# Kernel tuning notes

Measured on AMD Instinct MI355X. Metric: run time of the kernel, lower is better.

## Reference

```python
import jax, jax.numpy as jnp
import numpy as np

D_MODEL = 1024
NUM_HEADS = 16
HEAD_DIM = D_MODEL // NUM_HEADS
DILATION = 2
SEGMENT = 1024
OFFSET = 0  # head_idx % dilation_rate; head_idx derived from a random param in torch, fixed to 0 here


def setup_inputs() -> dict:
    key = jax.random.key(0)
    x = jax.random.normal(key, (4, 8192, D_MODEL), dtype=jnp.float32)
    return {"x": x}


def reference(x):
    b, n, d = x.shape  # n is already a multiple of SEGMENT (no padding needed)
    n_seg = n // SEGMENT
    k = SEGMENT // DILATION  # sparse tokens kept per segment

    # dilated gather: within each segment keep every DILATION-th token
    local_idx = OFFSET + DILATION * jnp.arange(k)                      # [k]
    global_idx = SEGMENT * jnp.arange(n_seg)[:, None] + local_idx[None, :]  # [n_seg, k]
    xs = x[:, global_idx, :]                                           # [b, n_seg, k, d]

    # multi-head self-attention within each sparse segment (q = k = v = xs)
    qh = xs.reshape(b, n_seg, k, NUM_HEADS, HEAD_DIM)
    scale = 1.0 / jnp.sqrt(jnp.asarray(HEAD_DIM, dtype=xs.dtype))
    scores = jnp.einsum('bsqhd,bskhd->bshqk', qh, qh) * scale          # [b, n_seg, h, k, k]
    attn = jax.nn.softmax(scores, axis=-1)
    seg_out = jnp.einsum('bshqk,bskhd->bsqhd', attn, qh)
    a_os = seg_out.reshape(b, n_seg * k, d)                            # [b, M, d]

    # mix_outputs: denominator-weighted scatter-add merge back to full sequence
    idx = jnp.broadcast_to(global_idx.reshape(-1), (b, n_seg * k))     # [b, M] global positions
    a_denoms = a_os.sum(axis=-1)                                       # [b, M]

    def mix(o_b, den_b, idx_b):
        sums = jnp.zeros((n,), o_b.dtype).at[idx_b].add(den_b)         # scatter_add of denoms
        alphas = den_b / sums[idx_b]                                   # gather + divide
        return jnp.zeros((n, d), o_b.dtype).at[idx_b].add(o_b * alphas[:, None])

    return jax.vmap(mix)(a_os, a_denoms, idx)                          # [b, n, d]
```

## Files before the change

### kernel.cpp

```cpp
#include <hip/hip_runtime.h>

#define DM 1024
#define NSEQ 8192

typedef __attribute__((ext_vector_type(8))) short short8;
typedef __attribute__((ext_vector_type(4))) float floatx4;

__device__ __forceinline__ unsigned pk_rn(float a, float b) {
  return __builtin_amdgcn_perm(__float_as_uint(b) + 0x8000u,
                               __float_as_uint(a) + 0x8000u, 0x07060302u);
}


__device__ __forceinline__ void build_vt(uint4* smem, int tid, int c, int buf) {
  const unsigned short* Ts = (const unsigned short*)smem;
  uint4* vb = &smem[4096 + buf * 1024];
  #pragma unroll
  for (int p = 0; p < 2; ++p) {
    int m = p * 512 + tid;
    int u16 = m >> 6, dp = m & 63;
    int d = dp ^ (u16 & 7);
    unsigned v[8];
    #pragma unroll
    for (int j = 0; j < 8; ++j) {
      int kk = c * 128 + 8 * u16 + j;
      v[j] = Ts[(kk * 8 + ((d >> 3) ^ j)) * 8 + (d & 7)];
    }
    uint4 pk;
    pk.x = v[0] | (v[1] << 16);
    pk.y = v[2] | (v[3] << 16);
    pk.z = v[4] | (v[5] << 16);
    pk.w = v[6] | (v[7] << 16);
    vb[m] = pk;
  }
}

__global__ __launch_bounds__(512, 2)
void fused_kernel(const float* __restrict__ x, float* __restrict__ out) {
  __shared__ uint4 smem[7168];
  const int tau = blockIdx.x;
  const int b = tau >> 7, s = (tau >> 4) & 7, h = tau & 15;
  const float* xb = x + ((size_t)b * NSEQ + s * 1024) * DM + h * 64;
  float* ob = out + ((size_t)b * NSEQ + s * 1024) * DM + h * 64;
  const int tid = threadIdx.x;
  const int lane = tid & 63;
  const int wu = __builtin_amdgcn_readfirstlane(tid >> 6);

  {
    const int c8 = tid & 7, rr = tid >> 3;
    float4 A[8], B[8];
    #pragma unroll
    for (int p = 0; p < 8; ++p) {
      int r = p * 64 + rr;
      const float* src = xb + (size_t)(2 * r) * DM + c8 * 8;
      A[p] = *(const float4*)src;
      B[p] = *(const float4*)(src + 4);
    }
    const float4 z = make_float4(0.f, 0.f, 0.f, 0.f);
    #pragma unroll
    for (int p = 0; p < 8; ++p) {
      int r = p * 64 + rr;
      float* zp = ob + (size_t)(2 * r + 1) * DM + c8 * 8;
      *(float4*)zp = z;
      *(float4*)(zp + 4) = z;
    }
    #pragma unroll
    for (int p = 0; p < 8; ++p) {
      int r = p * 64 + rr;
      uint4 pk;
      pk.x = pk_rn(A[p].x, A[p].y); pk.y = pk_rn(A[p].z, A[p].w);
      pk.z = pk_rn(B[p].x, B[p].y); pk.w = pk_rn(B[p].z, B[p].w);
      smem[r * 8 + (c8 ^ (r & 7))] = pk;
    }
  }
  __syncthreads();

  const int cq = lane & 15, u = lane >> 4;
  const int qw0 = wu * 64;

  short8 qf[4][2];
  #pragma unroll
  for (int qs = 0; qs < 4; ++qs) {
    int R = qw0 + qs * 16 + cq;
    #pragma unroll
    for (int ksd = 0; ksd < 2; ++ksd)
      qf[qs][ksd] = *(const short8*)&smem[R * 8 + ((4 * ksd + u) ^ (cq & 7))];
  }

  build_vt(smem, tid, 0, 0);
  __syncthreads();

  floatx4 o[4][4];
  #pragma unroll
  for (int qs = 0; qs < 4; ++qs)
    #pragma unroll
    for (int nt = 0; nt < 4; ++nt) o[qs][nt] = (floatx4){0.f, 0.f, 0.f, 0.f};
  float l[4] = {0.f, 0.f, 0.f, 0.f};
  const float cf = 0.125f * 1.44269504088896340736f;

  unsigned short* Pw = (unsigned short*)&smem[6144 + wu * 128];
  const int pswz = u ^ (cq & 3);

  for (int c = 0; c < 4; ++c) {
    if (c < 3) build_vt(smem, tid, c + 1, (c + 1) & 1);
    const uint4* vbase = &smem[4096 + (c & 1) * 1024];

    #pragma unroll
    for (int ks = 0; ks < 4; ++ks) {
      floatx4 acc[4][2];
      #pragma unroll
      for (int qs = 0; qs < 4; ++qs)
        #pragma unroll
        for (int t = 0; t < 2; ++t) acc[qs][t] = (floatx4){0.f, 0.f, 0.f, 0.f};
      #pragma unroll
      for (int t = 0; t < 2; ++t) {
        int R = c * 128 + 32 * ks + 16 * t + cq;
        #pragma unroll
        for (int ksd = 0; ksd < 2; ++ksd) {
          short8 af = *(short8*)&smem[R * 8 + ((4 * ksd + u) ^ (cq & 7))];
          #pragma unroll
          for (int qs = 0; qs < 4; ++qs)
            acc[qs][t] = __builtin_amdgcn_mfma_f32_16x16x32_bf16(af, qf[qs][ksd], acc[qs][t], 0, 0, 0);
        }
      }
      const int u16 = 4 * ks + u;
      short8 vfr[4];
      #pragma unroll
      for (int nt = 0; nt < 4; ++nt)
        vfr[nt] = *(const short8*)&vbase[u16 * 64 + 16 * nt + (cq ^ (u16 & 7))];
      #pragma unroll
      for (int qp = 0; qp < 2; ++qp) {
        #pragma unroll
        for (int q2 = 0; q2 < 2; ++q2) {
          int qs = 2 * qp + q2;
          #pragma unroll
          for (int t = 0; t < 2; ++t) {
            float p0 = __builtin_amdgcn_exp2f(acc[qs][t][0] * cf);
            float p1 = __builtin_amdgcn_exp2f(acc[qs][t][1] * cf);
            float p2 = __builtin_amdgcn_exp2f(acc[qs][t][2] * cf);
            float p3 = __builtin_amdgcn_exp2f(acc[qs][t][3] * cf);
            l[qs] += (p0 + p1) + (p2 + p3);
            uint2 w2;
            w2.x = pk_rn(p0, p1);
            w2.y = pk_rn(p2, p3);
            int unit = (q2 * 16 + cq) * 4 + ((2 * t + (u >> 1)) ^ (cq & 3));
            *(uint2*)(Pw + unit * 8 + (u & 1) * 4) = w2;
          }
        }
        #pragma unroll
        for (int q2 = 0; q2 < 2; ++q2) {
          int qs = 2 * qp + q2;
          short8 pf = *(short8*)(Pw + ((q2 * 16 + cq) * 4 + pswz) * 8);
          #pragma unroll
          for (int nt = 0; nt < 4; ++nt)
            o[qs][nt] = __builtin_amdgcn_mfma_f32_16x16x32_bf16(pf, vfr[nt], o[qs][nt], 0, 0, 0);
        }
      }
    }
    if (c < 3) __syncthreads();
  }

  #pragma unroll
  for (int qs = 0; qs < 4; ++qs) {
    float lf = l[qs];
    lf += __shfl_xor(lf, 16, 64);
    lf += __shfl_xor(lf, 32, 64);
    #pragma unroll
    for (int r = 0; r < 4; ++r) {
      float linv = 1.f / __shfl(lf, 4 * u + r, 64);
      float* orow = ob + (size_t)(2 * (qw0 + qs * 16 + 4 * u + r)) * DM + cq;
      #pragma unroll
      for (int nt = 0; nt < 4; ++nt)
        orow[nt * 16] = o[qs][nt][r] * linv;
    }
  }
}

extern "C" void kernel_launch(void* const* d_in, const int* in_sizes, int n_in,
                              void* d_out, int out_size, void* d_ws, size_t ws_size,
                              hipStream_t stream) {
  const float* x = (const float*)d_in[0];
  float* out = (float*)d_out;
  fused_kernel<<<dim3(512), dim3(512), 0, stream>>>(x, out);
}
```

Before: 293.5 us.

## Split each head-segment across two blocks with streamed double-buffered key chunks

Each (batch, segment, head) tile is now handled by two blocks, each owning half the query rows, so the grid doubles to 1024 blocks. Shared memory drops from 7168 to 4096 uint4 by keeping only two 128-row key chunks resident and streaming the rest from global memory into registers during compute. Launch bounds move to 4 blocks per CU. Each half starts at a different key chunk so the two blocks do not read the same chunk at the same time. The cost is that both halves read the full key/value set, doubling global reads of x, plus an extra barrier per chunk.

```diff
diff --git a/kernel.cpp b/kernel.cpp
--- a/kernel.cpp
+++ b/kernel.cpp
@@ -11,10 +11,8 @@
                                __float_as_uint(a) + 0x8000u, 0x07060302u);
 }
 
-
-__device__ __forceinline__ void build_vt(uint4* smem, int tid, int c, int buf) {
-  const unsigned short* Ts = (const unsigned short*)smem;
-  uint4* vb = &smem[4096 + buf * 1024];
+__device__ __forceinline__ void build_vt(uint4* smem, int tid, int bufsel) {
+  const unsigned short* Bs = (const unsigned short*)&smem[bufsel * 1024];
   #pragma unroll
   for (int p = 0; p < 2; ++p) {
     int m = p * 512 + tid;
@@ -23,103 +21,119 @@
     unsigned v[8];
     #pragma unroll
     for (int j = 0; j < 8; ++j) {
-      int kk = c * 128 + 8 * u16 + j;
-      v[j] = Ts[(kk * 8 + ((d >> 3) ^ j)) * 8 + (d & 7)];
+      int kkl = 8 * u16 + j;
+      v[j] = Bs[(kkl * 8 + ((d >> 3) ^ j)) * 8 + (d & 7)];
     }
     uint4 pk;
     pk.x = v[0] | (v[1] << 16);
     pk.y = v[2] | (v[3] << 16);
     pk.z = v[4] | (v[5] << 16);
     pk.w = v[6] | (v[7] << 16);
-    vb[m] = pk;
-  }
-}
-
-__global__ __launch_bounds__(512, 2)
-void fused_kernel(const float* __restrict__ x, float* __restrict__ out) {
-  __shared__ uint4 smem[7168];
-  const int tau = blockIdx.x;
+    smem[2048 + m] = pk;
+  }
+}
+
+__global__ __launch_bounds__(512, 4)
+void fused2(const float* __restrict__ x, float* __restrict__ out) {
+  __shared__ uint4 smem[4096];
+  const int g = blockIdx.x;
+  const int tau = (g & 7) * 64 + (g >> 4);
+  const int half = (g >> 3) & 1;
   const int b = tau >> 7, s = (tau >> 4) & 7, h = tau & 15;
   const float* xb = x + ((size_t)b * NSEQ + s * 1024) * DM + h * 64;
   float* ob = out + ((size_t)b * NSEQ + s * 1024) * DM + h * 64;
+  const int qoff = half * 256;
+  const int first = half * 2;
   const int tid = threadIdx.x;
   const int lane = tid & 63;
   const int wu = __builtin_amdgcn_readfirstlane(tid >> 6);
-
+  const int c8 = tid & 7, rr = tid >> 3;
+
+  float4 A[4], B[4];
+  #pragma unroll
+  for (int i = 0; i < 4; ++i) {
+    int rl = (i & 1) * 64 + rr;
+    int ch = first + (i >> 1);
+    const float* src = xb + (size_t)(2 * (128 * ch + rl)) * DM + c8 * 8;
+    A[i] = *(const float4*)src;
+    B[i] = *(const float4*)(src + 4);
+  }
   {
-    const int c8 = tid & 7, rr = tid >> 3;
-    float4 A[8], B[8];
-    #pragma unroll
-    for (int p = 0; p < 8; ++p) {
-      int r = p * 64 + rr;
-      const float* src = xb + (size_t)(2 * r) * DM + c8 * 8;
-      A[p] = *(const float4*)src;
-      B[p] = *(const float4*)(src + 4);
-    }
     const float4 z = make_float4(0.f, 0.f, 0.f, 0.f);
     #pragma unroll
-    for (int p = 0; p < 8; ++p) {
-      int r = p * 64 + rr;
-      float* zp = ob + (size_t)(2 * r + 1) * DM + c8 * 8;
+    for (int p = 0; p < 4; ++p) {
+      int j = qoff + p * 64 + rr;
+      float* zp = ob + (size_t)(2 * j + 1) * DM + c8 * 8;
       *(float4*)zp = z;
       *(float4*)(zp + 4) = z;
     }
-    #pragma unroll
-    for (int p = 0; p < 8; ++p) {
-      int r = p * 64 + rr;
-      uint4 pk;
-      pk.x = pk_rn(A[p].x, A[p].y); pk.y = pk_rn(A[p].z, A[p].w);
-      pk.z = pk_rn(B[p].x, B[p].y); pk.w = pk_rn(B[p].z, B[p].w);
-      smem[r * 8 + (c8 ^ (r & 7))] = pk;
-    }
+  }
+  #pragma unroll
+  for (int i = 0; i < 4; ++i) {
+    int rl = (i & 1) * 64 + rr;
+    uint4 pk;
+    pk.x = pk_rn(A[i].x, A[i].y); pk.y = pk_rn(A[i].z, A[i].w);
+    pk.z = pk_rn(B[i].x, B[i].y); pk.w = pk_rn(B[i].z, B[i].w);
+    smem[(i >> 1) * 1024 + rl * 8 + (c8 ^ (rl & 7))] = pk;
   }
   __syncthreads();
 
   const int cq = lane & 15, u = lane >> 4;
-  const int qw0 = wu * 64;
-
-  short8 qf[4][2];
-  #pragma unroll
-  for (int qs = 0; qs < 4; ++qs) {
-    int R = qw0 + qs * 16 + cq;
-    #pragma unroll
-    for (int ksd = 0; ksd < 2; ++ksd)
-      qf[qs][ksd] = *(const short8*)&smem[R * 8 + ((4 * ksd + u) ^ (cq & 7))];
-  }
-
-  build_vt(smem, tid, 0, 0);
+
+  short8 qf[2][2];
+  {
+    const uint4* bq = &smem[(wu >> 2) * 1024];
+    #pragma unroll
+    for (int qs = 0; qs < 2; ++qs) {
+      int rl = (wu & 3) * 32 + qs * 16 + cq;
+      #pragma unroll
+      for (int ksd = 0; ksd < 2; ++ksd)
+        qf[qs][ksd] = *(const short8*)&bq[rl * 8 + ((4 * ksd + u) ^ (cq & 7))];
+    }
+  }
+  build_vt(smem, tid, 0);
   __syncthreads();
 
-  floatx4 o[4][4];
-  #pragma unroll
-  for (int qs = 0; qs < 4; ++qs)
+  floatx4 o[2][4];
+  #pragma unroll
+  for (int qs = 0; qs < 2; ++qs)
     #pragma unroll
     for (int nt = 0; nt < 4; ++nt) o[qs][nt] = (floatx4){0.f, 0.f, 0.f, 0.f};
-  float l[4] = {0.f, 0.f, 0.f, 0.f};
+  float l[2] = {0.f, 0.f};
   const float cf = 0.125f * 1.44269504088896340736f;
 
-  unsigned short* Pw = (unsigned short*)&smem[6144 + wu * 128];
+  unsigned short* Pw = (unsigned short*)&smem[3072 + wu * 128];
   const int pswz = u ^ (cq & 3);
 
+  #pragma unroll
   for (int c = 0; c < 4; ++c) {
-    if (c < 3) build_vt(smem, tid, c + 1, (c + 1) & 1);
-    const uint4* vbase = &smem[4096 + (c & 1) * 1024];
+    float4 sA0, sB0, sA1, sB1;
+    if (c < 2) {
+      int ch = (first + c + 2) & 3;
+      const float* src0 = xb + (size_t)(2 * (128 * ch + rr)) * DM + c8 * 8;
+      sA0 = *(const float4*)src0;
+      sB0 = *(const float4*)(src0 + 4);
+      const float* src1 = xb + (size_t)(2 * (128 * ch + rr + 64)) * DM + c8 * 8;
+      sA1 = *(const float4*)src1;
+      sB1 = *(const float4*)(src1 + 4);
+    }
+    const uint4* kb = &smem[(c & 1) * 1024];
 
     #pragma unroll
     for (int ks = 0; ks < 4; ++ks) {
-      floatx4 acc[4][2];
-      #pragma unroll
-      for (int qs = 0; qs < 4; ++qs)
+      floatx4 acc[2][2];
+      #pragma unroll
+      for (int qs = 0; qs < 2; ++qs)
         #pragma unroll
         for (int t = 0; t < 2; ++t) acc[qs][t] = (floatx4){0.f, 0.f, 0.f, 0.f};
       #pragma unroll
       for (int t = 0; t < 2; ++t) {
-        int R = c * 128 + 32 * ks + 16 * t + cq;
+        int r = 32 * ks + 16 * t + cq;
         #pragma unroll
         for (int ksd = 0; ksd < 2; ++ksd) {
-          short8 af = *(short8*)&smem[R * 8 + ((4 * ksd + u) ^ (cq & 7))];
+          short8 af = *(const short8*)&kb[r * 8 + ((4 * ksd + u) ^ (cq & 7))];
           #pragma unroll
-          for (int qs = 0; qs < 4; ++qs)
+          for (int qs = 0; qs < 2; ++qs)
             acc[qs][t] = __builtin_amdgcn_mfma_f32_16x16x32_bf16(af, qf[qs][ksd], acc[qs][t], 0, 0, 0);
         }
       }
@@ -127,48 +141,58 @@
       short8 vfr[4];
       #pragma unroll
       for (int nt = 0; nt < 4; ++nt)
-        vfr[nt] = *(const short8*)&vbase[u16 * 64 + 16 * nt + (cq ^ (u16 & 7))];
-      #pragma unroll
-      for (int qp = 0; qp < 2; ++qp) {
-        #pragma unroll
-        for (int q2 = 0; q2 < 2; ++q2) {
-          int qs = 2 * qp + q2;
-          #pragma unroll
-          for (int t = 0; t < 2; ++t) {
-            float p0 = __builtin_amdgcn_exp2f(acc[qs][t][0] * cf);
-            float p1 = __builtin_amdgcn_exp2f(acc[qs][t][1] * cf);
-            float p2 = __builtin_amdgcn_exp2f(acc[qs][t][2] * cf);
-            float p3 = __builtin_amdgcn_exp2f(acc[qs][t][3] * cf);
-            l[qs] += (p0 + p1) + (p2 + p3);
-            uint2 w2;
-            w2.x = pk_rn(p0, p1);
-            w2.y = pk_rn(p2, p3);
-            int unit = (q2 * 16 + cq) * 4 + ((2 * t + (u >> 1)) ^ (cq & 3));
-            *(uint2*)(Pw + unit * 8 + (u & 1) * 4) = w2;
-          }
+        vfr[nt] = *(const short8*)&smem[2048 + u16 * 64 + 16 * nt + (cq ^ (u16 & 7))];
+      #pragma unroll
+      for (int qs = 0; qs < 2; ++qs)
+        #pragma unroll
+        for (int t = 0; t < 2; ++t) {
+          float p0 = __builtin_amdgcn_exp2f(acc[qs][t][0] * cf);
+          float p1 = __builtin_amdgcn_exp2f(acc[qs][t][1] * cf);
+          float p2 = __builtin_amdgcn_exp2f(acc[qs][t][2] * cf);
+          float p3 = __builtin_amdgcn_exp2f(acc[qs][t][3] * cf);
+          l[qs] += (p0 + p1) + (p2 + p3);
+          uint2 w2;
+          w2.x = pk_rn(p0, p1);
+          w2.y = pk_rn(p2, p3);
+          int unit = (qs * 16 + cq) * 4 + ((2 * t + (u >> 1)) ^ (cq & 3));
+          *(uint2*)(Pw + unit * 8 + (u & 1) * 4) = w2;
         }
-        #pragma unroll
-        for (int q2 = 0; q2 < 2; ++q2) {
-          int qs = 2 * qp + q2;
-          short8 pf = *(short8*)(Pw + ((q2 * 16 + cq) * 4 + pswz) * 8);
-          #pragma unroll
-          for (int nt = 0; nt < 4; ++nt)
-            o[qs][nt] = __builtin_amdgcn_mfma_f32_16x16x32_bf16(pf, vfr[nt], o[qs][nt], 0, 0, 0);
-        }
+      #pragma unroll
+      for (int qs = 0; qs < 2; ++qs) {
+        short8 pf = *(short8*)(Pw + ((qs * 16 + cq) * 4 + pswz) * 8);
+        #pragma unroll
+        for (int nt = 0; nt < 4; ++nt)
+          o[qs][nt] = __builtin_amdgcn_mfma_f32_16x16x32_bf16(pf, vfr[nt], o[qs][nt], 0, 0, 0);
       }
     }
-    if (c < 3) __syncthreads();
-  }
-
-  #pragma unroll
-  for (int qs = 0; qs < 4; ++qs) {
+
+    if (c < 3) {
+      __syncthreads();
+      if (c < 2) {
+        uint4 p0, p1;
+        p0.x = pk_rn(sA0.x, sA0.y); p0.y = pk_rn(sA0.z, sA0.w);
+        p0.z = pk_rn(sB0.x, sB0.y); p0.w = pk_rn(sB0.z, sB0.w);
+        p1.x = pk_rn(sA1.x, sA1.y); p1.y = pk_rn(sA1.z, sA1.w);
+        p1.z = pk_rn(sB1.x, sB1.y); p1.w = pk_rn(sB1.z, sB1.w);
+        uint4* kw = &smem[(c & 1) * 1024];
+        kw[rr * 8 + (c8 ^ (rr & 7))] = p0;
+        kw[(rr + 64) * 8 + (c8 ^ (rr & 7))] = p1;
+      }
+      build_vt(smem, tid, (c + 1) & 1);
+      __syncthreads();
+    }
+  }
+
+  #pragma unroll
+  for (int qs = 0; qs < 2; ++qs) {
     float lf = l[qs];
     lf += __shfl_xor(lf, 16, 64);
     lf += __shfl_xor(lf, 32, 64);
     #pragma unroll
     for (int r = 0; r < 4; ++r) {
       float linv = 1.f / __shfl(lf, 4 * u + r, 64);
-      float* orow = ob + (size_t)(2 * (qw0 + qs * 16 + 4 * u + r)) * DM + cq;
+      int qrow = qoff + wu * 32 + qs * 16 + 4 * u + r;
+      float* orow = ob + (size_t)(2 * qrow) * DM + cq;
       #pragma unroll
       for (int nt = 0; nt < 4; ++nt)
         orow[nt * 16] = o[qs][nt][r] * linv;
@@ -181,5 +205,5 @@
                               hipStream_t stream) {
   const float* x = (const float*)d_in[0];
   float* out = (float*)d_out;
-  fused_kernel<<<dim3(512), dim3(512), 0, stream>>>(x, out);
-}
+  fused2<<<dim3(1024), dim3(512), 0, stream>>>(x, out);
+}
```

After: 405.5 us. 38.1% more time.

## Stream K chunks through shared memory double buffer to cut LDS footprint

Applied to the files above, without the earlier changes.

Instead of staging the whole 512-row bf16 segment in LDS (112 KB), the kernel keeps only two 128-row K chunks plus one V-transpose buffer and the P scratch (64 KB), loading later chunks from global memory into registers during compute. Queries are loaded directly from global into registers. The launch bound is raised to 4 blocks per CU to improve occupancy. The cost is extra barriers per chunk, a V transpose that is no longer overlapped with compute, and more register pressure under a tighter register budget.

```diff
diff --git a/kernel.cpp b/kernel.cpp
--- a/kernel.cpp
+++ b/kernel.cpp
@@ -11,10 +11,8 @@
                                __float_as_uint(a) + 0x8000u, 0x07060302u);
 }
 
-
-__device__ __forceinline__ void build_vt(uint4* smem, int tid, int c, int buf) {
-  const unsigned short* Ts = (const unsigned short*)smem;
-  uint4* vb = &smem[4096 + buf * 1024];
+__device__ __forceinline__ void build_vt(uint4* smem, int tid, int bufsel) {
+  const unsigned short* Bs = (const unsigned short*)&smem[bufsel * 1024];
   #pragma unroll
   for (int p = 0; p < 2; ++p) {
     int m = p * 512 + tid;
@@ -23,21 +21,21 @@
     unsigned v[8];
     #pragma unroll
     for (int j = 0; j < 8; ++j) {
-      int kk = c * 128 + 8 * u16 + j;
-      v[j] = Ts[(kk * 8 + ((d >> 3) ^ j)) * 8 + (d & 7)];
+      int kkl = 8 * u16 + j;
+      v[j] = Bs[(kkl * 8 + ((d >> 3) ^ j)) * 8 + (d & 7)];
     }
     uint4 pk;
     pk.x = v[0] | (v[1] << 16);
     pk.y = v[2] | (v[3] << 16);
     pk.z = v[4] | (v[5] << 16);
     pk.w = v[6] | (v[7] << 16);
-    vb[m] = pk;
-  }
-}
-
-__global__ __launch_bounds__(512, 2)
-void fused_kernel(const float* __restrict__ x, float* __restrict__ out) {
-  __shared__ uint4 smem[7168];
+    smem[2048 + m] = pk;
+  }
+}
+
+__global__ __launch_bounds__(512, 4)
+void fused4(const float* __restrict__ x, float* __restrict__ out) {
+  __shared__ uint4 smem[4096];
   const int tau = blockIdx.x;
   const int b = tau >> 7, s = (tau >> 4) & 7, h = tau & 15;
   const float* xb = x + ((size_t)b * NSEQ + s * 1024) * DM + h * 64;
@@ -45,16 +43,35 @@
   const int tid = threadIdx.x;
   const int lane = tid & 63;
   const int wu = __builtin_amdgcn_readfirstlane(tid >> 6);
+  const int c8 = tid & 7, rr = tid >> 3;
+  const int cq = lane & 15, u = lane >> 4;
+  const int qw0 = wu * 64;
+
+  short8 qf[4][2];
+  #pragma unroll
+  for (int qs = 0; qs < 4; ++qs) {
+    const float* xq = xb + (size_t)(2 * (qw0 + qs * 16 + cq)) * DM;
+    #pragma unroll
+    for (int ksd = 0; ksd < 2; ++ksd) {
+      float4 a = *(const float4*)(xq + 32 * ksd + 8 * u);
+      float4 bq = *(const float4*)(xq + 32 * ksd + 8 * u + 4);
+      union { unsigned u4[4]; short8 s8; } pk;
+      pk.u4[0] = pk_rn(a.x, a.y);  pk.u4[1] = pk_rn(a.z, a.w);
+      pk.u4[2] = pk_rn(bq.x, bq.y); pk.u4[3] = pk_rn(bq.z, bq.w);
+      qf[qs][ksd] = pk.s8;
+    }
+  }
 
   {
-    const int c8 = tid & 7, rr = tid >> 3;
-    float4 A[8], B[8];
-    #pragma unroll
-    for (int p = 0; p < 8; ++p) {
-      int r = p * 64 + rr;
-      const float* src = xb + (size_t)(2 * r) * DM + c8 * 8;
-      A[p] = *(const float4*)src;
-      B[p] = *(const float4*)(src + 4);
+    uint4 st[4];
+    #pragma unroll
+    for (int i = 0; i < 4; ++i) {
+      int rl = (i & 1) * 64 + rr;
+      const float* src = xb + (size_t)(2 * (128 * (i >> 1) + rl)) * DM + c8 * 8;
+      float4 a = *(const float4*)src;
+      float4 bb = *(const float4*)(src + 4);
+      st[i].x = pk_rn(a.x, a.y);  st[i].y = pk_rn(a.z, a.w);
+      st[i].z = pk_rn(bb.x, bb.y); st[i].w = pk_rn(bb.z, bb.w);
     }
     const float4 z = make_float4(0.f, 0.f, 0.f, 0.f);
     #pragma unroll
@@ -65,29 +82,13 @@
       *(float4*)(zp + 4) = z;
     }
     #pragma unroll
-    for (int p = 0; p < 8; ++p) {
-      int r = p * 64 + rr;
-      uint4 pk;
-      pk.x = pk_rn(A[p].x, A[p].y); pk.y = pk_rn(A[p].z, A[p].w);
-      pk.z = pk_rn(B[p].x, B[p].y); pk.w = pk_rn(B[p].z, B[p].w);
-      smem[r * 8 + (c8 ^ (r & 7))] = pk;
+    for (int i = 0; i < 4; ++i) {
+      int rl = (i & 1) * 64 + rr;
+      smem[(i >> 1) * 1024 + rl * 8 + (c8 ^ (rl & 7))] = st[i];
     }
   }
   __syncthreads();
-
-  const int cq = lane & 15, u = lane >> 4;
-  const int qw0 = wu * 64;
-
-  short8 qf[4][2];
-  #pragma unroll
-  for (int qs = 0; qs < 4; ++qs) {
-    int R = qw0 + qs * 16 + cq;
-    #pragma unroll
-    for (int ksd = 0; ksd < 2; ++ksd)
-      qf[qs][ksd] = *(const short8*)&smem[R * 8 + ((4 * ksd + u) ^ (cq & 7))];
-  }
-
-  build_vt(smem, tid, 0, 0);
+  build_vt(smem, tid, 0);
   __syncthreads();
 
   floatx4 o[4][4];
@@ -98,12 +99,23 @@
   float l[4] = {0.f, 0.f, 0.f, 0.f};
   const float cf = 0.125f * 1.44269504088896340736f;
 
-  unsigned short* Pw = (unsigned short*)&smem[6144 + wu * 128];
+  unsigned short* Pw = (unsigned short*)&smem[3072 + wu * 128];
   const int pswz = u ^ (cq & 3);
 
   for (int c = 0; c < 4; ++c) {
-    if (c < 3) build_vt(smem, tid, c + 1, (c + 1) & 1);
-    const uint4* vbase = &smem[4096 + (c & 1) * 1024];
+    uint4 stg[2];
+    if (c < 2) {
+      #pragma unroll
+      for (int half = 0; half < 2; ++half) {
+        int rl = half * 64 + rr;
+        const float* src = xb + (size_t)(2 * (128 * (c + 2) + rl)) * DM + c8 * 8;
+        float4 a = *(const float4*)src;
+        float4 bb = *(const float4*)(src + 4);
+        stg[half].x = pk_rn(a.x, a.y);  stg[half].y = pk_rn(a.z, a.w);
+        stg[half].z = pk_rn(bb.x, bb.y); stg[half].w = pk_rn(bb.z, bb.w);
+      }
+    }
+    const uint4* kb = &smem[(c & 1) * 1024];
 
     #pragma unroll
     for (int ks = 0; ks < 4; ++ks) {
@@ -114,10 +126,10 @@
         for (int t = 0; t < 2; ++t) acc[qs][t] = (floatx4){0.f, 0.f, 0.f, 0.f};
       #pragma unroll
       for (int t = 0; t < 2; ++t) {
-        int R = c * 128 + 32 * ks + 16 * t + cq;
+        int r = 32 * ks + 16 * t + cq;
         #pragma unroll
         for (int ksd = 0; ksd < 2; ++ksd) {
-          short8 af = *(short8*)&smem[R * 8 + ((4 * ksd + u) ^ (cq & 7))];
+          short8 af = *(const short8*)&kb[r * 8 + ((4 * ksd + u) ^ (cq & 7))];
           #pragma unroll
           for (int qs = 0; qs < 4; ++qs)
             acc[qs][t] = __builtin_amdgcn_mfma_f32_16x16x32_bf16(af, qf[qs][ksd], acc[qs][t], 0, 0, 0);
@@ -127,7 +139,7 @@
       short8 vfr[4];
       #pragma unroll
       for (int nt = 0; nt < 4; ++nt)
-        vfr[nt] = *(const short8*)&vbase[u16 * 64 + 16 * nt + (cq ^ (u16 & 7))];
+        vfr[nt] = *(const short8*)&smem[2048 + u16 * 64 + 16 * nt + (cq ^ (u16 & 7))];
       #pragma unroll
       for (int qp = 0; qp < 2; ++qp) {
         #pragma unroll
@@ -157,7 +169,19 @@
         }
       }
     }
-    if (c < 3) __syncthreads();
+
+    if (c < 3) {
+      __syncthreads();
+      if (c < 2) {
+        #pragma unroll
+        for (int half = 0; half < 2; ++half) {
+          int rl = half * 64 + rr;
+          smem[(c & 1) * 1024 + rl * 8 + (c8 ^ (rl & 7))] = stg[half];
+        }
+      }
+      build_vt(smem, tid, (c + 1) & 1);
+      __syncthreads();
+    }
   }
 
   #pragma unroll
@@ -168,7 +192,8 @@
     #pragma unroll
     for (int r = 0; r < 4; ++r) {
       float linv = 1.f / __shfl(lf, 4 * u + r, 64);
-      float* orow = ob + (size_t)(2 * (qw0 + qs * 16 + 4 * u + r)) * DM + cq;
+      int qrow = qw0 + qs * 16 + 4 * u + r;
+      float* orow = ob + (size_t)(2 * qrow) * DM + cq;
       #pragma unroll
       for (int nt = 0; nt < 4; ++nt)
         orow[nt * 16] = o[qs][nt][r] * linv;
@@ -181,5 +206,5 @@
                               hipStream_t stream) {
   const float* x = (const float*)d_in[0];
   float* out = (float*)d_out;
-  fused_kernel<<<dim3(512), dim3(512), 0, stream>>>(x, out);
-}
+  fused4<<<dim3(512), dim3(512), 0, stream>>>(x, out);
+}
```

New measurement: 759.7 us. +158.8%, slower.
